# Performance work log

Hardware: AMD Instinct MI355X
Metric: run time of the kernel (lower is better)

Reference implementation:

```python
import jax, jax.numpy as jnp
import numpy as np

K_SELECT = 100      # select_box_nums_for_evaluation
IOU_THR = 0.7       # nms_iou_threshold
CONF_THR = 0.3      # confidence_score


def setup_inputs() -> dict:
    key = jax.random.key(0)
    k1, k2, k3 = jax.random.split(key, 3)
    B, Q, C = 256, 900, 91
    pred_logits = jax.random.normal(k1, (B, Q, C), dtype=jnp.float32)
    # cxcywh boxes in (0,1), strictly positive w/h
    pred_boxes = jax.random.uniform(k2, (B, Q, 4), dtype=jnp.float32, minval=0.05, maxval=0.45)
    # (img_h, img_w) per image
    target_sizes = jax.random.uniform(k3, (B, 2), dtype=jnp.float32, minval=200.0, maxval=1000.0)
    return {"pred_logits": pred_logits, "pred_boxes": pred_boxes, "target_sizes": target_sizes}


def _pairwise_iou(boxes):
    # boxes: [K,4] xyxy -> iou [K,K]
    area = (boxes[:, 2] - boxes[:, 0]) * (boxes[:, 3] - boxes[:, 1])
    lt = jnp.maximum(boxes[:, None, :2], boxes[None, :, :2])
    rb = jnp.minimum(boxes[:, None, 2:], boxes[None, :, 2:])
    wh = jnp.clip(rb - lt, 0.0)
    inter = wh[..., 0] * wh[..., 1]
    union = area[:, None] + area[None, :] - inter
    return inter / jnp.maximum(union, 1e-9)


def _nms_mask(boxes):
    # boxes already sorted by descending score (top_k output order).
    # Greedy NMS: box i suppresses lower-scored j if iou > IOU_THR and i itself kept.
    K = boxes.shape[0]
    iou = _pairwise_iou(boxes)
    rng = jnp.arange(K)

    def body(i, keep):
        suppress = (iou[i] > IOU_THR) & keep[i] & (rng > i)
        return keep & ~suppress

    return jax.lax.fori_loop(0, K, body, jnp.ones((K,), dtype=bool))


def reference(pred_logits, pred_boxes, target_sizes):
    B, Q, C = pred_logits.shape
    prob = jax.nn.sigmoid(pred_logits).reshape(B, Q * C)
    scores, topk_idx = jax.lax.top_k(prob, K_SELECT)        # [B,K] sorted desc
    topk_boxes = topk_idx // C                               # query index
    labels = topk_idx % C                                    # class index

    # cxcywh -> xyxy
    cxcy, wh = pred_boxes[..., :2], pred_boxes[..., 2:]
    xyxy = jnp.concatenate([cxcy - 0.5 * wh, cxcy + 0.5 * wh], axis=-1)  # [B,Q,4]
    boxes = jnp.take_along_axis(xyxy, topk_boxes[..., None], axis=1)     # [B,K,4]

    img_h, img_w = target_sizes[:, 0], target_sizes[:, 1]
    scale_fct = jnp.stack([img_w, img_h, img_w, img_h], axis=1)          # [B,4]
    boxes = boxes * scale_fct[:, None, :]

    conf_keep = scores > CONF_THR                            # confidence filter
    nms_keep = jax.vmap(_nms_mask)(boxes)                    # per-image NMS
    keep = conf_keep & nms_keep                              # fixed-shape mask (ragged lists in torch)
    return scores, labels, boxes, keep
```

## Files before the change

kernel.cpp:

```cpp
#include <hip/hip_runtime.h>
#include <stdint.h>

#define NBATCH 256
#define NQ 900
#define NC 91
#define NQC (NQ * NC)
#define NV4 (NQC / 4)
#define KSEL 100
#define IOU_THRF 0.7f
#define CONF_THRF 0.3f
#define TH_LOGIT 2.2f
#define DELTA 4096u

#define NT 1024
#define CAPB 2048
#define HBINS 64
#define SRTCAP 512

__device__ __forceinline__ uint32_t fkey(float x) {
  uint32_t b = __float_as_uint(x);
  return b ^ ((uint32_t)((int32_t)b >> 31) | 0x80000000u);
}
__device__ __forceinline__ float unfkey(uint32_t k) {
  uint32_t b = (k & 0x80000000u) ? (k ^ 0x80000000u) : ~k;
  return __uint_as_float(b);
}
__device__ __forceinline__ float sigmoidf_ref(float x) {
  return 1.0f / (1.0f + expf(-x));
}

union SMem {
  struct {
    unsigned long long keys[CAPB];
    unsigned long long srt[SRTCAP];
  } p;
  struct {
    float iou[KSEL * KSEL];
    float box[KSEL][4];
    int keep[KSEL];
  } nms;
};

__global__ __launch_bounds__(NT) void postproc(const float* __restrict__ logits,
                                               const float* __restrict__ pboxes,
                                               const float* __restrict__ tsizes,
                                               float* __restrict__ out) {
  __shared__ SMem sm;
  __shared__ unsigned long long rankbuf[KSEL];
  __shared__ uint32_t s_hist[HBINS];
  __shared__ uint32_t s_lcnt, s_cut, s_m;
  __shared__ unsigned long long red[NT / 64];
  __shared__ unsigned long long s_last;

  const int b = blockIdx.x;
  const int tid = threadIdx.x;
  const float* lg = logits + (size_t)b * NQC;
  const float4* lg4 = (const float4*)lg;

  if (tid == 0) s_lcnt = 0;
  __syncthreads();

#define PROC4(v, ii)                                                           \
  {                                                                            \
    const uint32_t ibase = (uint32_t)((ii) * 4);                               \
    if ((v).x >= TH_LOGIT) {                                                   \
      uint32_t p = atomicAdd(&s_lcnt, 1u);                                     \
      if (p < CAPB) sm.p.keys[p] = (((unsigned long long)fkey((v).x)) << 32) | (ibase + 0); \
    }                                                                          \
    if ((v).y >= TH_LOGIT) {                                                   \
      uint32_t p = atomicAdd(&s_lcnt, 1u);                                     \
      if (p < CAPB) sm.p.keys[p] = (((unsigned long long)fkey((v).y)) << 32) | (ibase + 1); \
    }                                                                          \
    if ((v).z >= TH_LOGIT) {                                                   \
      uint32_t p = atomicAdd(&s_lcnt, 1u);                                     \
      if (p < CAPB) sm.p.keys[p] = (((unsigned long long)fkey((v).z)) << 32) | (ibase + 2); \
    }                                                                          \
    if ((v).w >= TH_LOGIT) {                                                   \
      uint32_t p = atomicAdd(&s_lcnt, 1u);                                     \
      if (p < CAPB) sm.p.keys[p] = (((unsigned long long)fkey((v).w)) << 32) | (ibase + 3); \
    }                                                                          \
  }

  {
    const float4 z4 = make_float4(0.f, 0.f, 0.f, 0.f);
    for (int i = tid; i < NV4; i += 4 * NT) {
      const bool g1 = (i + NT) < NV4;
      const bool g2 = (i + 2 * NT) < NV4;
      const bool g3 = (i + 3 * NT) < NV4;
      const float4 a0 = lg4[i];
      const float4 a1 = g1 ? lg4[i + NT] : z4;
      const float4 a2 = g2 ? lg4[i + 2 * NT] : z4;
      const float4 a3 = g3 ? lg4[i + 3 * NT] : z4;
      PROC4(a0, i)
      PROC4(a1, i + NT)
      PROC4(a2, i + 2 * NT)
      PROC4(a3, i + 3 * NT)
    }
  }
#undef PROC4

  __syncthreads();
  const uint32_t n = s_lcnt;
  bool good = (n >= KSEL && n <= CAPB);

  if (good) {
    if (tid < HBINS) s_hist[tid] = 0;
    if (tid == 0) s_m = 0;
    __syncthreads();

    for (uint32_t i = tid; i < n; i += NT) {
      uint32_t k = (uint32_t)(sm.p.keys[i] >> 32);
      uint32_t bin = (k >> 20) - 0xC00u;
      if (bin > HBINS - 1) bin = HBINS - 1;
      atomicAdd(&s_hist[bin], 1u);
    }
    __syncthreads();

    if (tid < 64) {
      uint32_t h = s_hist[tid];
      uint32_t suf = h;
      #pragma unroll
      for (int off = 1; off < 64; off <<= 1) {
        uint32_t t = __shfl_down(suf, off);
        if (tid + off < 64) suf += t;
      }
      bool pred = (suf >= KSEL) && (suf - h < KSEL);
      unsigned long long mask = __ballot(pred);
      int cutlane = __ffsll((long long)mask) - 1;
      if (tid == 0) s_cut = (uint32_t)cutlane;
    }
    __syncthreads();
    const uint32_t cut = s_cut;
    if (cut >= HBINS - 1) good = false;
    const uint32_t thresh = ((cut + 0xC00u) << 20) - DELTA;

    if (good) {
      for (uint32_t i = tid; i < n; i += NT) {
        unsigned long long key = sm.p.keys[i];
        uint32_t k = (uint32_t)(key >> 32);
        if (k >= thresh) {
          uint32_t pb = __float_as_uint(sigmoidf_ref(unfkey(k)));
          uint32_t pos = atomicAdd(&s_m, 1u);
          if (pos < SRTCAP)
            sm.p.srt[pos] = (((unsigned long long)(~pb)) << 32) |
                            (key & 0xFFFFFFFFULL);
        }
      }
      __syncthreads();
      const uint32_t m = s_m;
      if (m > SRTCAP) good = false;
      if (good) {
        for (uint32_t q = tid; q < m; q += NT) {
          unsigned long long mykey = sm.p.srt[q];
          uint32_t r = 0;
          for (uint32_t j = 0; j < m; j++)
            r += (sm.p.srt[j] < mykey) ? 1u : 0u;
          if (r < KSEL) rankbuf[r] = mykey;
        }
        __syncthreads();
      }
    }
  }

  if (!good) {
    unsigned long long last = ~0ULL;
    for (int r = 0; r < KSEL; r++) {
      unsigned long long best = 0ULL;
      for (int i = tid; i < NQC; i += NT) {
        uint32_t pb = __float_as_uint(sigmoidf_ref(lg[i]));
        unsigned long long cmp = (((unsigned long long)pb) << 32) |
                                 (unsigned long long)(~(uint32_t)i);
        if (cmp < last && cmp > best) best = cmp;
      }
      #pragma unroll
      for (int o = 32; o >= 1; o >>= 1) {
        unsigned long long other = __shfl_down(best, o);
        if (other > best) best = other;
      }
      if ((tid & 63) == 0) red[tid >> 6] = best;
      __syncthreads();
      if (tid == 0) {
        unsigned long long mx = red[0];
        for (int w = 1; w < NT / 64; w++) if (red[w] > mx) mx = red[w];
        s_last = mx;
        uint32_t pb = (uint32_t)(mx >> 32);
        uint32_t id = ~(uint32_t)mx;
        rankbuf[r] = (((unsigned long long)(~pb)) << 32) | (unsigned long long)id;
      }
      __syncthreads();
      last = s_last;
    }
  }

  float score = 0.0f;
  int idx = 0;
  if (tid < KSEL) {
    unsigned long long key = rankbuf[tid];
    score = __uint_as_float(~(uint32_t)(key >> 32));
    idx = (int)(uint32_t)(key & 0xFFFFFFFFu);
  }
  __syncthreads();

  const float img_h = tsizes[b * 2 + 0];
  const float img_w = tsizes[b * 2 + 1];
  float* out_scores = out;
  float* out_labels = out + (size_t)NBATCH * KSEL;
  float* out_boxes  = out + (size_t)2 * NBATCH * KSEL;
  float* out_keep   = out + (size_t)2 * NBATCH * KSEL + (size_t)NBATCH * KSEL * 4;

  if (tid < KSEL) {
    int q = idx / NC;
    int lab = idx - q * NC;
    const float* pb = pboxes + ((size_t)b * NQ + q) * 4;
    float cx = pb[0], cy = pb[1], w = pb[2], h = pb[3];
    float hw = __fmul_rn(0.5f, w), hh = __fmul_rn(0.5f, h);
    float x0 = __fmul_rn(__fsub_rn(cx, hw), img_w);
    float y0 = __fmul_rn(__fsub_rn(cy, hh), img_h);
    float x1 = __fmul_rn(__fadd_rn(cx, hw), img_w);
    float y1 = __fmul_rn(__fadd_rn(cy, hh), img_h);
    out_scores[(size_t)b * KSEL + tid] = score;
    out_labels[(size_t)b * KSEL + tid] = (float)lab;
    float* ob = out_boxes + ((size_t)b * KSEL + tid) * 4;
    ob[0] = x0; ob[1] = y0; ob[2] = x1; ob[3] = y1;
    sm.nms.box[tid][0] = x0; sm.nms.box[tid][1] = y0;
    sm.nms.box[tid][2] = x1; sm.nms.box[tid][3] = y1;
  }
  __syncthreads();

  for (int e = tid; e < KSEL * KSEL; e += NT) {
    int i = e / KSEL;
    int j = e - i * KSEL;
    float ax0 = sm.nms.box[i][0], ay0 = sm.nms.box[i][1];
    float ax1 = sm.nms.box[i][2], ay1 = sm.nms.box[i][3];
    float bx0 = sm.nms.box[j][0], by0 = sm.nms.box[j][1];
    float bx1 = sm.nms.box[j][2], by1 = sm.nms.box[j][3];
    float areaA = __fmul_rn(__fsub_rn(ax1, ax0), __fsub_rn(ay1, ay0));
    float areaB = __fmul_rn(__fsub_rn(bx1, bx0), __fsub_rn(by1, by0));
    float ltx = fmaxf(ax0, bx0), lty = fmaxf(ay0, by0);
    float rbx = fminf(ax1, bx1), rby = fminf(ay1, by1);
    float wx = fmaxf(__fsub_rn(rbx, ltx), 0.0f);
    float wy = fmaxf(__fsub_rn(rby, lty), 0.0f);
    float inter = __fmul_rn(wx, wy);
    float uni = __fsub_rn(__fadd_rn(areaA, areaB), inter);
    sm.nms.iou[e] = __fdiv_rn(inter, fmaxf(uni, 1e-9f));
  }
  __syncthreads();

  if (tid < 64) {
    int keepA = 1;
    int keepB = 1;
    for (int i = 0; i < KSEL; i++) {
      int owner = i & 63;
      int ki = (i < 64) ? __shfl(keepA, owner) : __shfl(keepB, owner);
      if (ki) {
        if (tid > i && sm.nms.iou[i * KSEL + tid] > IOU_THRF) keepA = 0;
        int j = tid + 64;
        if (j < KSEL && j > i && sm.nms.iou[i * KSEL + j] > IOU_THRF) keepB = 0;
      }
    }
    sm.nms.keep[tid] = keepA;
    if (tid + 64 < KSEL) sm.nms.keep[tid + 64] = keepB;
  }
  __syncthreads();

  if (tid < KSEL) {
    float kp = (score > CONF_THRF && sm.nms.keep[tid]) ? 1.0f : 0.0f;
    out_keep[(size_t)b * KSEL + tid] = kp;
  }
}

extern "C" void kernel_launch(void* const* d_in, const int* in_sizes, int n_in,
                              void* d_out, int out_size, void* d_ws, size_t ws_size,
                              hipStream_t stream) {
  const float* logits = (const float*)d_in[0];
  const float* pboxes = (const float*)d_in[1];
  const float* tsizes = (const float*)d_in[2];
  (void)in_sizes; (void)n_in; (void)out_size; (void)d_ws; (void)ws_size;
  postproc<<<NBATCH, NT, 0, stream>>>(logits, pboxes, tsizes, (float*)d_out);
}
```

Baseline: 44.01 us.

## Stage logits into LDS via global_load_lds in chunked passes

Replaces the direct per-thread float4 global loads of the logit scan with asynchronous global-to-LDS loads into a 4096-float4 staging buffer, processed in five chunks with barriers between them. The staging buffer is unioned with the sort and NMS scratch, while the candidate key array is now kept separate. The aim is to make the global-read stream more efficient. The cost is extra LDS traffic, a synchronisation per chunk, no overlap between loading and filtering, and a larger LDS footprint.

Result: slower. 51.13 us (+16.2%).

```diff
diff --git a/kernel.cpp b/kernel.cpp
--- a/kernel.cpp
+++ b/kernel.cpp
@@ -13,6 +13,9 @@
 #define DELTA 4096u
 
 #define NT 1024
+#define NWAVE (NT / 64)
+#define CHUNK_F4 4096
+#define NCHUNK 5
 #define CAPB 2048
 #define HBINS 64
 #define SRTCAP 512
@@ -29,31 +32,34 @@
   return 1.0f / (1.0f + expf(-x));
 }
 
-union SMem {
-  struct {
-    unsigned long long keys[CAPB];
+struct SMemT {
+  unsigned long long keys[CAPB];
+  union {
+    float4 stage[CHUNK_F4];
     unsigned long long srt[SRTCAP];
-  } p;
-  struct {
-    float iou[KSEL * KSEL];
-    float box[KSEL][4];
-    int keep[KSEL];
-  } nms;
+    struct {
+      float iou[KSEL * KSEL];
+      float box[KSEL][4];
+      int keep[KSEL];
+    } nms;
+  } u;
 };
 
 __global__ __launch_bounds__(NT) void postproc(const float* __restrict__ logits,
                                                const float* __restrict__ pboxes,
                                                const float* __restrict__ tsizes,
                                                float* __restrict__ out) {
-  __shared__ SMem sm;
+  __shared__ SMemT sm;
   __shared__ unsigned long long rankbuf[KSEL];
   __shared__ uint32_t s_hist[HBINS];
   __shared__ uint32_t s_lcnt, s_cut, s_m;
-  __shared__ unsigned long long red[NT / 64];
+  __shared__ unsigned long long red[NWAVE];
   __shared__ unsigned long long s_last;
 
   const int b = blockIdx.x;
   const int tid = threadIdx.x;
+  const int w = tid >> 6;
+  const int lane = tid & 63;
   const float* lg = logits + (size_t)b * NQC;
   const float4* lg4 = (const float4*)lg;
 
@@ -65,36 +71,41 @@
     const uint32_t ibase = (uint32_t)((ii) * 4);                               \
     if ((v).x >= TH_LOGIT) {                                                   \
       uint32_t p = atomicAdd(&s_lcnt, 1u);                                     \
-      if (p < CAPB) sm.p.keys[p] = (((unsigned long long)fkey((v).x)) << 32) | (ibase + 0); \
+      if (p < CAPB) sm.keys[p] = (((unsigned long long)fkey((v).x)) << 32) | (ibase + 0); \
     }                                                                          \
     if ((v).y >= TH_LOGIT) {                                                   \
       uint32_t p = atomicAdd(&s_lcnt, 1u);                                     \
-      if (p < CAPB) sm.p.keys[p] = (((unsigned long long)fkey((v).y)) << 32) | (ibase + 1); \
+      if (p < CAPB) sm.keys[p] = (((unsigned long long)fkey((v).y)) << 32) | (ibase + 1); \
     }                                                                          \
     if ((v).z >= TH_LOGIT) {                                                   \
       uint32_t p = atomicAdd(&s_lcnt, 1u);                                     \
-      if (p < CAPB) sm.p.keys[p] = (((unsigned long long)fkey((v).z)) << 32) | (ibase + 2); \
+      if (p < CAPB) sm.keys[p] = (((unsigned long long)fkey((v).z)) << 32) | (ibase + 2); \
     }                                                                          \
     if ((v).w >= TH_LOGIT) {                                                   \
       uint32_t p = atomicAdd(&s_lcnt, 1u);                                     \
-      if (p < CAPB) sm.p.keys[p] = (((unsigned long long)fkey((v).w)) << 32) | (ibase + 3); \
-    }                                                                          \
-  }
-
-  {
-    const float4 z4 = make_float4(0.f, 0.f, 0.f, 0.f);
-    for (int i = tid; i < NV4; i += 4 * NT) {
-      const bool g1 = (i + NT) < NV4;
-      const bool g2 = (i + 2 * NT) < NV4;
-      const bool g3 = (i + 3 * NT) < NV4;
-      const float4 a0 = lg4[i];
-      const float4 a1 = g1 ? lg4[i + NT] : z4;
-      const float4 a2 = g2 ? lg4[i + 2 * NT] : z4;
-      const float4 a3 = g3 ? lg4[i + 3 * NT] : z4;
-      PROC4(a0, i)
-      PROC4(a1, i + NT)
-      PROC4(a2, i + 2 * NT)
-      PROC4(a3, i + 3 * NT)
+      if (p < CAPB) sm.keys[p] = (((unsigned long long)fkey((v).w)) << 32) | (ibase + 3); \
+    }                                                                          \
+  }
+
+  for (int c = 0; c < NCHUNK; ++c) {
+    if (c > 0) __syncthreads();
+    #pragma unroll
+    for (int j = 0; j < 4; ++j) {
+      const int slot = w * 256 + j * 64;
+      int gi = c * CHUNK_F4 + slot + lane;
+      if (gi > NV4 - 1) gi = NV4 - 1;
+      __builtin_amdgcn_global_load_lds(
+          (const __attribute__((address_space(1))) void*)(lg4 + gi),
+          (__attribute__((address_space(3))) void*)(&sm.u.stage[slot]),
+          16, 0, 0);
+    }
+    __syncthreads();
+    for (int s = tid; s < CHUNK_F4; s += NT) {
+      const int f4i = c * CHUNK_F4 + s;
+      if (f4i < NV4) {
+        const float4 v = sm.u.stage[s];
+        PROC4(v, f4i)
+      }
     }
   }
 #undef PROC4
@@ -109,7 +120,7 @@
     __syncthreads();
 
     for (uint32_t i = tid; i < n; i += NT) {
-      uint32_t k = (uint32_t)(sm.p.keys[i] >> 32);
+      uint32_t k = (uint32_t)(sm.keys[i] >> 32);
       uint32_t bin = (k >> 20) - 0xC00u;
       if (bin > HBINS - 1) bin = HBINS - 1;
       atomicAdd(&s_hist[bin], 1u);
@@ -136,13 +147,13 @@
 
     if (good) {
       for (uint32_t i = tid; i < n; i += NT) {
-        unsigned long long key = sm.p.keys[i];
+        unsigned long long key = sm.keys[i];
         uint32_t k = (uint32_t)(key >> 32);
         if (k >= thresh) {
           uint32_t pb = __float_as_uint(sigmoidf_ref(unfkey(k)));
           uint32_t pos = atomicAdd(&s_m, 1u);
           if (pos < SRTCAP)
-            sm.p.srt[pos] = (((unsigned long long)(~pb)) << 32) |
+            sm.u.srt[pos] = (((unsigned long long)(~pb)) << 32) |
                             (key & 0xFFFFFFFFULL);
         }
       }
@@ -151,10 +162,10 @@
       if (m > SRTCAP) good = false;
       if (good) {
         for (uint32_t q = tid; q < m; q += NT) {
-          unsigned long long mykey = sm.p.srt[q];
+          unsigned long long mykey = sm.u.srt[q];
           uint32_t r = 0;
           for (uint32_t j = 0; j < m; j++)
-            r += (sm.p.srt[j] < mykey) ? 1u : 0u;
+            r += (sm.u.srt[j] < mykey) ? 1u : 0u;
           if (r < KSEL) rankbuf[r] = mykey;
         }
         __syncthreads();
@@ -181,7 +192,7 @@
       __syncthreads();
       if (tid == 0) {
         unsigned long long mx = red[0];
-        for (int w = 1; w < NT / 64; w++) if (red[w] > mx) mx = red[w];
+        for (int ww = 1; ww < NWAVE; ww++) if (red[ww] > mx) mx = red[ww];
         s_last = mx;
         uint32_t pb = (uint32_t)(mx >> 32);
         uint32_t id = ~(uint32_t)mx;
@@ -212,8 +223,8 @@
     int q = idx / NC;
     int lab = idx - q * NC;
     const float* pb = pboxes + ((size_t)b * NQ + q) * 4;
-    float cx = pb[0], cy = pb[1], w = pb[2], h = pb[3];
-    float hw = __fmul_rn(0.5f, w), hh = __fmul_rn(0.5f, h);
+    float cx = pb[0], cy = pb[1], w4 = pb[2], h4 = pb[3];
+    float hw = __fmul_rn(0.5f, w4), hh = __fmul_rn(0.5f, h4);
     float x0 = __fmul_rn(__fsub_rn(cx, hw), img_w);
     float y0 = __fmul_rn(__fsub_rn(cy, hh), img_h);
     float x1 = __fmul_rn(__fadd_rn(cx, hw), img_w);
@@ -222,18 +233,18 @@
     out_labels[(size_t)b * KSEL + tid] = (float)lab;
     float* ob = out_boxes + ((size_t)b * KSEL + tid) * 4;
     ob[0] = x0; ob[1] = y0; ob[2] = x1; ob[3] = y1;
-    sm.nms.box[tid][0] = x0; sm.nms.box[tid][1] = y0;
-    sm.nms.box[tid][2] = x1; sm.nms.box[tid][3] = y1;
+    sm.u.nms.box[tid][0] = x0; sm.u.nms.box[tid][1] = y0;
+    sm.u.nms.box[tid][2] = x1; sm.u.nms.box[tid][3] = y1;
   }
   __syncthreads();
 
   for (int e = tid; e < KSEL * KSEL; e += NT) {
     int i = e / KSEL;
     int j = e - i * KSEL;
-    float ax0 = sm.nms.box[i][0], ay0 = sm.nms.box[i][1];
-    float ax1 = sm.nms.box[i][2], ay1 = sm.nms.box[i][3];
-    float bx0 = sm.nms.box[j][0], by0 = sm.nms.box[j][1];
-    float bx1 = sm.nms.box[j][2], by1 = sm.nms.box[j][3];
+    float ax0 = sm.u.nms.box[i][0], ay0 = sm.u.nms.box[i][1];
+    float ax1 = sm.u.nms.box[i][2], ay1 = sm.u.nms.box[i][3];
+    float bx0 = sm.u.nms.box[j][0], by0 = sm.u.nms.box[j][1];
+    float bx1 = sm.u.nms.box[j][2], by1 = sm.u.nms.box[j][3];
     float areaA = __fmul_rn(__fsub_rn(ax1, ax0), __fsub_rn(ay1, ay0));
     float areaB = __fmul_rn(__fsub_rn(bx1, bx0), __fsub_rn(by1, by0));
     float ltx = fmaxf(ax0, bx0), lty = fmaxf(ay0, by0);
@@ -242,7 +253,7 @@
     float wy = fmaxf(__fsub_rn(rby, lty), 0.0f);
     float inter = __fmul_rn(wx, wy);
     float uni = __fsub_rn(__fadd_rn(areaA, areaB), inter);
-    sm.nms.iou[e] = __fdiv_rn(inter, fmaxf(uni, 1e-9f));
+    sm.u.nms.iou[e] = __fdiv_rn(inter, fmaxf(uni, 1e-9f));
   }
   __syncthreads();
 
@@ -253,18 +264,18 @@
       int owner = i & 63;
       int ki = (i < 64) ? __shfl(keepA, owner) : __shfl(keepB, owner);
       if (ki) {
-        if (tid > i && sm.nms.iou[i * KSEL + tid] > IOU_THRF) keepA = 0;
+        if (tid > i && sm.u.nms.iou[i * KSEL + tid] > IOU_THRF) keepA = 0;
         int j = tid + 64;
-        if (j < KSEL && j > i && sm.nms.iou[i * KSEL + j] > IOU_THRF) keepB = 0;
-      }
-    }
-    sm.nms.keep[tid] = keepA;
-    if (tid + 64 < KSEL) sm.nms.keep[tid + 64] = keepB;
+        if (j < KSEL && j > i && sm.u.nms.iou[i * KSEL + j] > IOU_THRF) keepB = 0;
+      }
+    }
+    sm.u.nms.keep[tid] = keepA;
+    if (tid + 64 < KSEL) sm.u.nms.keep[tid + 64] = keepB;
   }
   __syncthreads();
 
   if (tid < KSEL) {
-    float kp = (score > CONF_THRF && sm.nms.keep[tid]) ? 1.0f : 0.0f;
+    float kp = (score > CONF_THRF && sm.u.nms.keep[tid]) ? 1.0f : 0.0f;
     out_keep[(size_t)b * KSEL + tid] = kp;
   }
 }
```
